# Kernel optimization log

Measured on AMD Instinct MI355X. Metric: run time of the kernel, lower is better.

Reference implementation:

```python
import jax, jax.numpy as jnp
import numpy as np

NOISE_LEVEL = 0.05
GAMMA = 0.2  # dt/tau


def setup_inputs() -> dict:
    key = jax.random.key(0)
    ks = jax.random.split(key, 4)
    B, T, I, L, O = 64, 512, 128, 1024, 128
    return {
        "input": jax.random.normal(ks[0], (B, T, I), dtype=jnp.float32),
        "noise": jax.random.normal(ks[1], (B, T, L), dtype=jnp.float32),
        "wi": jax.random.normal(ks[2], (I, L), dtype=jnp.float32),
        "si": jnp.ones((I,), dtype=jnp.float32),
        "wrec": jax.random.normal(ks[3], (L, L), dtype=jnp.float32) * (1.0 / np.sqrt(L)),
        "b": jnp.zeros((L,), dtype=jnp.float32),
        "wo": jax.random.normal(jax.random.fold_in(key, 7), (L, O), dtype=jnp.float32) * (1.0 / L),
        "so": jnp.ones((O,), dtype=jnp.float32),
        "h0": jnp.zeros((L,), dtype=jnp.float32),
    }


def reference(input, noise, wi, si, wrec, b, wo, so, h0):
    B = input.shape[0]
    # proxy parameters: wi_full = (wi.T * si).T == wi * si[:, None]; wo_full = wo * so
    wi_full = wi * si[:, None]          # (I, L)
    wo_full = wo * so                   # (L, O)

    h_init = jnp.broadcast_to(h0, (B, h0.shape[0]))  # (B, L)
    r_init = jnp.tanh(h_init)

    # Precompute input projections for all steps (no sequential dependency).
    u = jnp.einsum('bti,il->btl', input, wi_full)     # (B, T, L)

    def step(carry, xs):
        h, r = carry
        u_t, n_t = xs                                 # (B, L), (B, L)
        h = h + NOISE_LEVEL * n_t + GAMMA * (-h + r @ wrec.T + u_t)
        r = jnp.tanh(h + b)
        out_t = jnp.tanh(h) @ wo_full                 # (B, O)
        return (h, r), out_t

    xs = (jnp.swapaxes(u, 0, 1), jnp.swapaxes(noise, 0, 1))  # time-major
    _, out_t = jax.lax.scan(step, (h_init, r_init), xs)
    return jnp.swapaxes(out_t, 0, 1)                 # (B, T, O)
```

## Files before the change

### kernel.cpp

```cpp
#include <hip/hip_runtime.h>
#include <hip/hip_bf16.h>
#include <cstdint>
#include <cstddef>


static constexpr int B = 64, T = 512, I = 128, L = 1024, O = 128;
static constexpr float C_NOISE = 0.05f, C_GAMMA = 0.2f;

static constexpr int NROW = 4, BT = 16, NJB = 16, JT = 64;

static constexpr size_t WREC_OFF = 0;
static constexpr size_t WIT_OFF  = WREC_OFF + (size_t)L * L * 2;
static constexpr size_t WOT_OFF  = WIT_OFF + (size_t)L * I * 2;
static constexpr size_t RBUF_OFF = WOT_OFF + (size_t)O * L * 2;
static constexpr size_t FLAG_OFF = RBUF_OFF + (size_t)2 * B * L * 2;
static constexpr size_t NFLAGS   = (size_t)NROW * (T + 1) * NJB * 4;
static constexpr size_t FLAG_BYTES = NFLAGS * 4;
static constexpr size_t HBUF_OFF = ((FLAG_OFF + FLAG_BYTES + 511) / 512) * 512;
static constexpr size_t WS_NEED  = HBUF_OFF + (size_t)B * T * L * 2;

typedef __attribute__((ext_vector_type(8))) short s16x8;
typedef __attribute__((ext_vector_type(4))) float f32x4;
typedef __attribute__((ext_vector_type(2))) unsigned long long u64x2;
typedef __attribute__((ext_vector_type(4))) unsigned int u32x4;

__device__ __forceinline__ float fexp2(float x) {
#if __has_builtin(__builtin_amdgcn_exp2f)
  return __builtin_amdgcn_exp2f(x);
#else
  return exp2f(x);
#endif
}
__device__ __forceinline__ float frcp(float x) {
#if __has_builtin(__builtin_amdgcn_rcpf)
  return __builtin_amdgcn_rcpf(x);
#else
  return 1.0f / x;
#endif
}
__device__ __forceinline__ float fast_tanh(float x) {
  float e = fexp2(x * 2.8853900817779268f);
  return 1.0f - 2.0f * frcp(e + 1.0f);
}
__device__ __forceinline__ uint16_t bf16bits(float x) {
  __hip_bfloat16 h = __float2bfloat16(x);
  return *reinterpret_cast<uint16_t*>(&h);
}

__global__ void pack_kernel(const float* __restrict__ wi, const float* __restrict__ si,
                            const float* __restrict__ wrec,
                            const float* __restrict__ wo, const float* __restrict__ so,
                            uint8_t* __restrict__ ws) {
  int idx = blockIdx.x * blockDim.x + threadIdx.x;
  int stride = gridDim.x * blockDim.x;

  __hip_bfloat16* wrecb = (__hip_bfloat16*)(ws + WREC_OFF);
  for (int i = idx; i < L * L; i += stride) wrecb[i] = __float2bfloat16(wrec[i]);

  __hip_bfloat16* wit = (__hip_bfloat16*)(ws + WIT_OFF);
  for (int n = idx; n < L * I; n += stride) {
    int l = n >> 7, ii = n & 127;
    wit[n] = __float2bfloat16(wi[(size_t)ii * L + l] * si[ii]);
  }
  __hip_bfloat16* wot = (__hip_bfloat16*)(ws + WOT_OFF);
  for (int n = idx; n < O * L; n += stride) {
    int o = n >> 10, l = n & 1023;
    wot[n] = __float2bfloat16(wo[(size_t)l * O + o] * so[o]);
  }
  uint32_t* flags = (uint32_t*)(ws + FLAG_OFF);
  for (size_t n = idx; n < NFLAGS; n += stride) flags[n] = 0;
}

__launch_bounds__(256, 1)
__global__ void rnn_kernel(const float* __restrict__ input, const float* __restrict__ noise,
                           const float* __restrict__ bvec, const float* __restrict__ h0,
                           uint8_t* __restrict__ ws) {
  const int tid  = threadIdx.x;
  const int lane = tid & 63;
  const int w    = tid >> 6;
  const int bx   = blockIdx.x;
  const int row  = bx & 3;
  const int jblk = bx >> 2;
  const int b0   = row * BT;
  const int j0   = jblk * JT;
  const int l15  = lane & 15;
  const int lhi  = lane >> 4;
  const int jcol = j0 + w * 16 + l15;

  const short* wrecb = (const short*)(ws + WREC_OFF);
  const short* wit   = (const short*)(ws + WIT_OFF);
  uint64_t* rbuf     = (uint64_t*)(ws + RBUF_OFF);
  uint32_t* flags    = (uint32_t*)(ws + FLAG_OFF);
  __hip_bfloat16* hbuf = (__hip_bfloat16*)(ws + HBUF_OFF);

  __shared__ __align__(16) uint8_t ldsA[2][16 * 2048];
  __shared__ __align__(8)  __hip_bfloat16 ldsR[4 * 256];

  s16x8 wfrag[32];
  #pragma unroll
  for (int kt = 0; kt < 32; ++kt)
    wfrag[kt] = *(const s16x8*)(wrecb + (size_t)jcol * L + kt * 32 + lhi * 8);
  s16x8 wifrag[4];
  #pragma unroll
  for (int kt = 0; kt < 4; ++kt)
    wifrag[kt] = *(const s16x8*)(wit + (size_t)jcol * I + kt * 32 + lhi * 8);

  const float bias = bvec[jcol];
  float h[4];
  { float hv = h0[jcol]; h[0] = h[1] = h[2] = h[3] = hv; }

  const int grow = tid >> 4;
  const int gx   = tid & 15;
  const int gsw  = (grow ^ gx) & 7;
  const int pbb = lane >> 2;
  const int pcq = lane & 3;
  __hip_bfloat16* ldsRw = ldsR + w * 256;

  {
    uint64_t pv = 0;
    #pragma unroll
    for (int q = 0; q < 4; ++q)
      pv |= (uint64_t)bf16bits(fast_tanh(h0[j0 + w * 16 + pcq * 4 + q])) << (16 * q);
    size_t slot = (size_t)(b0 + pbb) * (L / 4) + (size_t)(j0 >> 2) + w * 4 + pcq;
    __hip_atomic_store(&rbuf[slot], pv, __ATOMIC_RELAXED, __HIP_MEMORY_SCOPE_AGENT);
    __builtin_amdgcn_s_waitcnt(0);
    if (lane == 0)
      __hip_atomic_store(&flags[((size_t)(row * (T + 1) + 0) * NJB + jblk) * 4 + w], 1u,
                         __ATOMIC_RELAXED, __HIP_MEMORY_SCOPE_AGENT);
  }

  for (int t = 0; t < T; ++t) {
    f32x4 inLo[4], inHi[4];
    #pragma unroll
    for (int kt = 0; kt < 4; ++kt) {
      const float* p = input + ((size_t)(b0 + l15) * T + t) * I + kt * 32 + lhi * 8;
      inLo[kt] = *(const f32x4*)p;
      inHi[kt] = *(const f32x4*)(p + 4);
    }
    float nz[4];
    #pragma unroll
    for (int q = 0; q < 4; ++q)
      nz[q] = noise[((size_t)(b0 + lhi * 4 + q) * T + t) * L + jcol];
    s16x8 af[4];
    #pragma unroll
    for (int kt = 0; kt < 4; ++kt)
      #pragma unroll
      for (int q = 0; q < 4; ++q) {
        af[kt][q]     = (short)bf16bits(inLo[kt][q]);
        af[kt][q + 4] = (short)bf16bits(inHi[kt][q]);
      }

    {
      const uint32_t* fp = flags + ((size_t)(row * (T + 1) + t) * NJB + gx) * 4;
      u32x4 f4;
      do {
        asm volatile("global_load_dwordx4 %0, %1, off sc0 sc1\n\ts_waitcnt vmcnt(0)"
                     : "=v"(f4) : "v"(fp) : "memory");
      } while ((f4.x & f4.y & f4.z & f4.w) == 0u);

      const uint8_t* src = (const uint8_t*)rbuf
                         + (size_t)(t & 1) * (B * L * 2)
                         + (size_t)(b0 + grow) * 2048 + (size_t)gx * 128;
      u64x2 v[8];
      #pragma unroll
      for (int i = 0; i < 8; ++i)
        asm volatile("global_load_dwordx4 %0, %1, off sc0 sc1"
                     : "=v"(v[i]) : "v"(src + i * 16) : "memory");
      asm volatile("s_waitcnt vmcnt(0)" ::: "memory");
      __builtin_amdgcn_sched_barrier(0);
      uint8_t* dst = ldsA[t & 1] + grow * 2048 + gx * 128;
      #pragma unroll
      for (int i = 0; i < 8; ++i)
        *(u64x2*)(dst + ((i ^ gsw) * 16)) = v[i];
    }
    __syncthreads();

    const uint8_t* Ab = ldsA[t & 1];
    f32x4 acc0 = {0.f, 0.f, 0.f, 0.f}, acc1 = {0.f, 0.f, 0.f, 0.f};
    #pragma unroll
    for (int kt = 0; kt < 32; ++kt) {
      int slot = ((kt * 4 + lhi) ^ ((l15 ^ (kt >> 1)) & 7)) * 16;
      s16x8 a = *(const s16x8*)(Ab + l15 * 2048 + slot);
      if (kt & 1) acc1 = __builtin_amdgcn_mfma_f32_16x16x32_bf16(a, wfrag[kt], acc1, 0, 0, 0);
      else        acc0 = __builtin_amdgcn_mfma_f32_16x16x32_bf16(a, wfrag[kt], acc0, 0, 0, 0);
    }
    #pragma unroll
    for (int kt = 0; kt < 4; ++kt) {
      if (kt & 1) acc1 = __builtin_amdgcn_mfma_f32_16x16x32_bf16(af[kt], wifrag[kt], acc1, 0, 0, 0);
      else        acc0 = __builtin_amdgcn_mfma_f32_16x16x32_bf16(af[kt], wifrag[kt], acc0, 0, 0, 0);
    }

    #pragma unroll
    for (int q = 0; q < 4; ++q) {
      float hn = 0.8f * h[q] + C_GAMMA * (acc0[q] + acc1[q]) + C_NOISE * nz[q];
      h[q] = hn;
      ldsRw[(lhi * 4 + q) * 16 + l15] = __float2bfloat16(fast_tanh(hn + bias));
    }

    {
      uint64_t pv = *(const uint64_t*)(ldsRw + pbb * 16 + pcq * 4);
      size_t slot = (size_t)((t + 1) & 1) * (B * L / 4)
                  + (size_t)(b0 + pbb) * (L / 4) + (size_t)(j0 >> 2) + w * 4 + pcq;
      __hip_atomic_store(&rbuf[slot], pv, __ATOMIC_RELAXED, __HIP_MEMORY_SCOPE_AGENT);
    }
    __builtin_amdgcn_s_waitcnt(0);
    if (lane == 0)
      __hip_atomic_store(&flags[((size_t)(row * (T + 1) + (t + 1)) * NJB + jblk) * 4 + w], 1u,
                         __ATOMIC_RELAXED, __HIP_MEMORY_SCOPE_AGENT);

    #pragma unroll
    for (int q = 0; q < 4; ++q)
      hbuf[((size_t)(b0 + lhi * 4 + q) * T + t) * L + jcol] = __float2bfloat16(fast_tanh(h[q]));
  }
}

__launch_bounds__(256)
__global__ void out_gemm(const uint8_t* __restrict__ ws, float* __restrict__ out) {
  const short* hs  = (const short*)(ws + HBUF_OFF);
  const short* wot = (const short*)(ws + WOT_OFF);
  const int tid = threadIdx.x, lane = tid & 63, w = tid >> 6;
  const int wm = w >> 1, wn = w & 1;
  const int l15 = lane & 15, lhi = lane >> 4;
  const size_t m0 = (size_t)blockIdx.x * 128 + (size_t)wm * 64;

  f32x4 acc[4][4] = {};
  for (int kt = 0; kt < 32; ++kt) {
    s16x8 a[4], b[4];
    #pragma unroll
    for (int fi = 0; fi < 4; ++fi)
      a[fi] = *(const s16x8*)(hs + (m0 + fi * 16 + l15) * L + kt * 32 + lhi * 8);
    #pragma unroll
    for (int fj = 0; fj < 4; ++fj)
      b[fj] = *(const s16x8*)(wot + (size_t)(wn * 64 + fj * 16 + l15) * L + kt * 32 + lhi * 8);
    #pragma unroll
    for (int fi = 0; fi < 4; ++fi)
      #pragma unroll
      for (int fj = 0; fj < 4; ++fj)
        acc[fi][fj] = __builtin_amdgcn_mfma_f32_16x16x32_bf16(a[fi], b[fj], acc[fi][fj], 0, 0, 0);
  }
  #pragma unroll
  for (int fi = 0; fi < 4; ++fi)
    #pragma unroll
    for (int fj = 0; fj < 4; ++fj)
      #pragma unroll
      for (int q = 0; q < 4; ++q) {
        size_t m = m0 + fi * 16 + lhi * 4 + q;
        out[m * O + wn * 64 + fj * 16 + l15] = acc[fi][fj][q];
      }
}

__global__ void ws_too_small(float* out, int n) {
  int i = blockIdx.x * blockDim.x + threadIdx.x;
  if (i < n) out[i] = 12345.0f;
}

extern "C" void kernel_launch(void* const* d_in, const int* in_sizes, int n_in,
                              void* d_out, int out_size, void* d_ws, size_t ws_size,
                              hipStream_t stream) {
  const float* input = (const float*)d_in[0];
  const float* noise = (const float*)d_in[1];
  const float* wi    = (const float*)d_in[2];
  const float* si    = (const float*)d_in[3];
  const float* wrec  = (const float*)d_in[4];
  const float* bvec  = (const float*)d_in[5];
  const float* wo    = (const float*)d_in[6];
  const float* so    = (const float*)d_in[7];
  const float* h0    = (const float*)d_in[8];
  uint8_t* ws = (uint8_t*)d_ws;
  float* out = (float*)d_out;

  if (ws_size < WS_NEED) {
    ws_too_small<<<(out_size + 255) / 256, 256, 0, stream>>>(out, out_size);
    return;
  }

  pack_kernel<<<256, 256, 0, stream>>>(wi, si, wrec, wo, so, ws);
  rnn_kernel<<<NROW * NJB, 256, 0, stream>>>(input, noise, bvec, h0, ws);
  out_gemm<<<(B * T) / 128, 256, 0, stream>>>(ws, out);
}
```

Measured before the change: 2.097 ms.

## Transpose MFMA operands so each lane owns 4 contiguous hidden units per batch

Swaps the A/B operands of the recurrent and input MFMAs so the accumulator layout gives each lane four consecutive hidden columns for one batch row. The packed bf16 r vector can then be built in registers and stored directly, which removes the LDS staging buffer. Noise loads and hbuf writes also become single vector accesses. The input-projection MFMAs are issued before the flag spin-wait so they overlap with waiting on other blocks, and four accumulators replace two to shorten MFMA dependency chains.

```diff
diff --git a/kernel.cpp b/kernel.cpp
--- a/kernel.cpp
+++ b/kernel.cpp
@@ -21,8 +21,8 @@
 
 typedef __attribute__((ext_vector_type(8))) short s16x8;
 typedef __attribute__((ext_vector_type(4))) float f32x4;
+typedef __attribute__((ext_vector_type(4))) unsigned int u32x4;
 typedef __attribute__((ext_vector_type(2))) unsigned long long u64x2;
-typedef __attribute__((ext_vector_type(4))) unsigned int u32x4;
 
 __device__ __forceinline__ float fexp2(float x) {
 #if __has_builtin(__builtin_amdgcn_exp2f)
@@ -85,7 +85,9 @@
   const int j0   = jblk * JT;
   const int l15  = lane & 15;
   const int lhi  = lane >> 4;
-  const int jcol = j0 + w * 16 + l15;
+
+  const int jc0  = j0 + w * 16 + lhi * 4;
+  const int mybatch = b0 + l15;
 
   const short* wrecb = (const short*)(ws + WREC_OFF);
   const short* wit   = (const short*)(ws + WIT_OFF);
@@ -94,34 +96,30 @@
   __hip_bfloat16* hbuf = (__hip_bfloat16*)(ws + HBUF_OFF);
 
   __shared__ __align__(16) uint8_t ldsA[2][16 * 2048];
-  __shared__ __align__(8)  __hip_bfloat16 ldsR[4 * 256];
 
   s16x8 wfrag[32];
   #pragma unroll
   for (int kt = 0; kt < 32; ++kt)
-    wfrag[kt] = *(const s16x8*)(wrecb + (size_t)jcol * L + kt * 32 + lhi * 8);
+    wfrag[kt] = *(const s16x8*)(wrecb + (size_t)(j0 + w * 16 + l15) * L + kt * 32 + lhi * 8);
   s16x8 wifrag[4];
   #pragma unroll
   for (int kt = 0; kt < 4; ++kt)
-    wifrag[kt] = *(const s16x8*)(wit + (size_t)jcol * I + kt * 32 + lhi * 8);
-
-  const float bias = bvec[jcol];
-  float h[4];
-  { float hv = h0[jcol]; h[0] = h[1] = h[2] = h[3] = hv; }
+    wifrag[kt] = *(const s16x8*)(wit + (size_t)(j0 + w * 16 + l15) * I + kt * 32 + lhi * 8);
+
+  f32x4 bias, h;
+  #pragma unroll
+  for (int q = 0; q < 4; ++q) { bias[q] = bvec[jc0 + q]; h[q] = h0[jc0 + q]; }
 
   const int grow = tid >> 4;
-  const int gx   = tid & 15;
-  const int gsw  = (grow ^ gx) & 7;
-  const int pbb = lane >> 2;
-  const int pcq = lane & 3;
-  __hip_bfloat16* ldsRw = ldsR + w * 256;
+  const int gseg = tid & 15;
+  const int gsw  = (grow ^ gseg) & 7;
 
   {
     uint64_t pv = 0;
     #pragma unroll
     for (int q = 0; q < 4; ++q)
-      pv |= (uint64_t)bf16bits(fast_tanh(h0[j0 + w * 16 + pcq * 4 + q])) << (16 * q);
-    size_t slot = (size_t)(b0 + pbb) * (L / 4) + (size_t)(j0 >> 2) + w * 4 + pcq;
+      pv |= (uint64_t)bf16bits(fast_tanh(h0[jc0 + q])) << (16 * q);
+    size_t slot = (size_t)mybatch * (L / 4) + (size_t)(jc0 >> 2);
     __hip_atomic_store(&rbuf[slot], pv, __ATOMIC_RELAXED, __HIP_MEMORY_SCOPE_AGENT);
     __builtin_amdgcn_s_waitcnt(0);
     if (lane == 0)
@@ -137,10 +135,7 @@
       inLo[kt] = *(const f32x4*)p;
       inHi[kt] = *(const f32x4*)(p + 4);
     }
-    float nz[4];
-    #pragma unroll
-    for (int q = 0; q < 4; ++q)
-      nz[q] = noise[((size_t)(b0 + lhi * 4 + q) * T + t) * L + jcol];
+    f32x4 nz = *(const f32x4*)(noise + ((size_t)mybatch * T + t) * L + jc0);
     s16x8 af[4];
     #pragma unroll
     for (int kt = 0; kt < 4; ++kt)
@@ -150,25 +145,34 @@
         af[kt][q + 4] = (short)bf16bits(inHi[kt][q]);
       }
 
-    {
-      const uint32_t* fp = flags + ((size_t)(row * (T + 1) + t) * NJB + gx) * 4;
+    f32x4 acc0 = {0.f,0.f,0.f,0.f}, acc1 = {0.f,0.f,0.f,0.f};
+    f32x4 acc2 = {0.f,0.f,0.f,0.f}, acc3 = {0.f,0.f,0.f,0.f};
+    acc0 = __builtin_amdgcn_mfma_f32_16x16x32_bf16(wifrag[0], af[0], acc0, 0, 0, 0);
+    acc1 = __builtin_amdgcn_mfma_f32_16x16x32_bf16(wifrag[1], af[1], acc1, 0, 0, 0);
+    acc2 = __builtin_amdgcn_mfma_f32_16x16x32_bf16(wifrag[2], af[2], acc2, 0, 0, 0);
+    acc3 = __builtin_amdgcn_mfma_f32_16x16x32_bf16(wifrag[3], af[3], acc3, 0, 0, 0);
+
+    {
+      const uint32_t* fp = flags + ((size_t)(row * (T + 1) + t) * NJB + gseg) * 4;
       u32x4 f4;
       do {
         asm volatile("global_load_dwordx4 %0, %1, off sc0 sc1\n\ts_waitcnt vmcnt(0)"
-                     : "=v"(f4) : "v"(fp) : "memory");
+                     : "=&v"(f4) : "v"(fp) : "memory");
       } while ((f4.x & f4.y & f4.z & f4.w) == 0u);
-
+    }
+
+    {
       const uint8_t* src = (const uint8_t*)rbuf
                          + (size_t)(t & 1) * (B * L * 2)
-                         + (size_t)(b0 + grow) * 2048 + (size_t)gx * 128;
+                         + (size_t)(b0 + grow) * 2048 + (size_t)gseg * 128;
       u64x2 v[8];
       #pragma unroll
       for (int i = 0; i < 8; ++i)
         asm volatile("global_load_dwordx4 %0, %1, off sc0 sc1"
-                     : "=v"(v[i]) : "v"(src + i * 16) : "memory");
+                     : "=&v"(v[i]) : "v"(src + i * 16) : "memory");
       asm volatile("s_waitcnt vmcnt(0)" ::: "memory");
       __builtin_amdgcn_sched_barrier(0);
-      uint8_t* dst = ldsA[t & 1] + grow * 2048 + gx * 128;
+      uint8_t* dst = ldsA[t & 1] + grow * 2048 + gseg * 128;
       #pragma unroll
       for (int i = 0; i < 8; ++i)
         *(u64x2*)(dst + ((i ^ gsw) * 16)) = v[i];
@@ -176,31 +180,29 @@
     __syncthreads();
 
     const uint8_t* Ab = ldsA[t & 1];
-    f32x4 acc0 = {0.f, 0.f, 0.f, 0.f}, acc1 = {0.f, 0.f, 0.f, 0.f};
     #pragma unroll
     for (int kt = 0; kt < 32; ++kt) {
       int slot = ((kt * 4 + lhi) ^ ((l15 ^ (kt >> 1)) & 7)) * 16;
       s16x8 a = *(const s16x8*)(Ab + l15 * 2048 + slot);
-      if (kt & 1) acc1 = __builtin_amdgcn_mfma_f32_16x16x32_bf16(a, wfrag[kt], acc1, 0, 0, 0);
-      else        acc0 = __builtin_amdgcn_mfma_f32_16x16x32_bf16(a, wfrag[kt], acc0, 0, 0, 0);
-    }
-    #pragma unroll
-    for (int kt = 0; kt < 4; ++kt) {
-      if (kt & 1) acc1 = __builtin_amdgcn_mfma_f32_16x16x32_bf16(af[kt], wifrag[kt], acc1, 0, 0, 0);
-      else        acc0 = __builtin_amdgcn_mfma_f32_16x16x32_bf16(af[kt], wifrag[kt], acc0, 0, 0, 0);
-    }
-
+      switch (kt & 3) {
+        case 0: acc0 = __builtin_amdgcn_mfma_f32_16x16x32_bf16(wfrag[kt], a, acc0, 0, 0, 0); break;
+        case 1: acc1 = __builtin_amdgcn_mfma_f32_16x16x32_bf16(wfrag[kt], a, acc1, 0, 0, 0); break;
+        case 2: acc2 = __builtin_amdgcn_mfma_f32_16x16x32_bf16(wfrag[kt], a, acc2, 0, 0, 0); break;
+        default: acc3 = __builtin_amdgcn_mfma_f32_16x16x32_bf16(wfrag[kt], a, acc3, 0, 0, 0); break;
+      }
+    }
+
+    uint64_t pv = 0;
     #pragma unroll
     for (int q = 0; q < 4; ++q) {
-      float hn = 0.8f * h[q] + C_GAMMA * (acc0[q] + acc1[q]) + C_NOISE * nz[q];
+      float hn = 0.8f * h[q] + C_GAMMA * ((acc0[q] + acc1[q]) + (acc2[q] + acc3[q]))
+               + C_NOISE * nz[q];
       h[q] = hn;
-      ldsRw[(lhi * 4 + q) * 16 + l15] = __float2bfloat16(fast_tanh(hn + bias));
-    }
-
-    {
-      uint64_t pv = *(const uint64_t*)(ldsRw + pbb * 16 + pcq * 4);
+      pv |= (uint64_t)bf16bits(fast_tanh(hn + bias[q])) << (16 * q);
+    }
+    {
       size_t slot = (size_t)((t + 1) & 1) * (B * L / 4)
-                  + (size_t)(b0 + pbb) * (L / 4) + (size_t)(j0 >> 2) + w * 4 + pcq;
+                  + (size_t)mybatch * (L / 4) + (size_t)(jc0 >> 2);
       __hip_atomic_store(&rbuf[slot], pv, __ATOMIC_RELAXED, __HIP_MEMORY_SCOPE_AGENT);
     }
     __builtin_amdgcn_s_waitcnt(0);
@@ -208,9 +210,13 @@
       __hip_atomic_store(&flags[((size_t)(row * (T + 1) + (t + 1)) * NJB + jblk) * 4 + w], 1u,
                          __ATOMIC_RELAXED, __HIP_MEMORY_SCOPE_AGENT);
 
-    #pragma unroll
-    for (int q = 0; q < 4; ++q)
-      hbuf[((size_t)(b0 + lhi * 4 + q) * T + t) * L + jcol] = __float2bfloat16(fast_tanh(h[q]));
+    {
+      uint64_t hv = 0;
+      #pragma unroll
+      for (int q = 0; q < 4; ++q)
+        hv |= (uint64_t)bf16bits(fast_tanh(h[q])) << (16 * q);
+      *(uint64_t*)(hbuf + ((size_t)mybatch * T + t) * L + jc0) = hv;
+    }
   }
 }
 
```

Measured after the change: 2.060 ms (median of 2 runs). About the same (-1.8%).
